# Performance work log

Hardware: AMD Instinct MI355X
Metric: run time of the kernel (lower is better)

## Reference

```python
import jax, jax.numpy as jnp
import numpy as np
import math

DIM = 512
HEADS = 8
DIM_HEAD = 64
INNER = HEADS * DIM_HEAD


def setup_inputs() -> dict:
    key = jax.random.key(0)
    k1, k2, k3, k4 = jax.random.split(key, 4)
    x = jax.random.normal(k1, (8, 1024, DIM), dtype=jnp.float32)
    w_qkv = jax.random.normal(k2, (DIM, INNER * 3), dtype=jnp.float32) / math.sqrt(DIM)
    w_out = jax.random.normal(k3, (INNER, DIM), dtype=jnp.float32) / math.sqrt(INNER)
    temperature = jnp.array(math.log(DIM_HEAD ** -0.5), dtype=jnp.float32)
    return {"x": x, "w_qkv": w_qkv, "w_out": w_out, "temperature": temperature}


def reference(x, w_qkv, w_out, temperature):
    b, n, _ = x.shape
    qkv = x @ w_qkv  # [b, n, 3*inner]
    q, k, v = jnp.split(qkv, 3, axis=-1)
    # [b, n, h*d] -> [b, h, n, d]
    def split_heads(t):
        return t.reshape(b, n, HEADS, DIM_HEAD).transpose(0, 2, 1, 3)
    q, k, v = split_heads(q), split_heads(k), split_heads(v)
    dots = jnp.einsum('bhnd,bhmd->bhnm', q, k) * jnp.exp(temperature)
    mask_value = -jnp.finfo(dots.dtype).max
    eye = jnp.eye(n, dtype=bool)
    dots = jnp.where(eye, mask_value, dots)
    attn = jax.nn.softmax(dots, axis=-1)
    out = jnp.einsum('bhnm,bhmd->bhnd', attn, v)
    out = out.transpose(0, 2, 1, 3).reshape(b, n, INNER)
    return out @ w_out
```

## Files before the change

kernel.cpp:

```cpp
#include <hip/hip_runtime.h>
#include <math.h>

#define BATCH  8
#define SEQ    1024
#define DMODEL 512
#define NHEADS 8
#define DHEAD  64
#define MTOT   (BATCH*SEQ)
#define QKVLD  (3*DMODEL)

typedef unsigned short ushortT;
typedef __attribute__((ext_vector_type(8))) short short8;
typedef __attribute__((ext_vector_type(4))) float f32x4;

typedef __attribute__((address_space(3))) unsigned char lds_byte;
typedef __attribute__((address_space(1))) const unsigned char glob_byte;

__device__ inline void g2l16(const void* g, void* l) {
    __builtin_amdgcn_global_load_lds((glob_byte*)g, (lds_byte*)l, 16, 0, 0);
}

__device__ inline ushortT f2bf(float f) {
    union { float f; unsigned u; } v; v.f = f;
    unsigned r = (v.u + 0x7FFFu + ((v.u >> 16) & 1u)) >> 16;
    return (ushortT)r;
}
__device__ inline ushortT f2bf_fast(float f) {
    union { float f; unsigned u; } v; v.f = f;
    return (ushortT)((v.u + 0x8000u) >> 16);
}

__global__ __launch_bounds__(256)
void cvt_bf16(const float* __restrict__ in, ushortT* __restrict__ out, int n8)
{
    int gid = blockIdx.x * 256 + threadIdx.x;
    if (gid >= n8) return;
    const float4 a = *(const float4*)(in + (long)gid*8);
    const float4 b = *(const float4*)(in + (long)gid*8 + 4);
    ushortT o[8];
    o[0]=f2bf(a.x); o[1]=f2bf(a.y); o[2]=f2bf(a.z); o[3]=f2bf(a.w);
    o[4]=f2bf(b.x); o[5]=f2bf(b.y); o[6]=f2bf(b.z); o[7]=f2bf(b.w);
    *(short8*)(out + (long)gid*8) = *(short8*)o;
}

__global__ __launch_bounds__(256)
void cvt_transpose2(const float* __restrict__ Wq, ushortT* __restrict__ WqT,
                    const float* __restrict__ Wo, ushortT* __restrict__ WoT)
{
    __shared__ float T[32][33];
    const int t = threadIdx.x;
    int bid = blockIdx.x;
    const float* W; ushortT* WT; int N, n0, k0;
    if (bid < 768) { W = Wq; WT = WqT; N = QKVLD;  n0 = (bid % 48) * 32; k0 = (bid / 48) * 32; }
    else { bid -= 768; W = Wo; WT = WoT; N = DMODEL; n0 = (bid % 16) * 32; k0 = (bid / 16) * 32; }
    const int K = DMODEL;
    {
        const int r = t >> 3, c4 = (t & 7) * 4;
        const float4 v = *(const float4*)(W + (long)(k0 + r)*N + n0 + c4);
        T[c4+0][r] = v.x; T[c4+1][r] = v.y; T[c4+2][r] = v.z; T[c4+3][r] = v.w;
    }
    __syncthreads();
    {
        const int n = t >> 3, k4 = (t & 7) * 4;
        ushortT o[4];
        o[0] = f2bf(T[n][k4+0]); o[1] = f2bf(T[n][k4+1]);
        o[2] = f2bf(T[n][k4+2]); o[3] = f2bf(T[n][k4+3]);
        *(uint2*)(WT + (long)(n0 + n)*K + k0 + k4) = *(uint2*)o;
    }
}

template <int MODE>
__global__ __launch_bounds__(256, 3)
void gemm_bf16(const ushortT* __restrict__ A, const ushortT* __restrict__ BT,
               void* __restrict__ Cv, ushortT* __restrict__ vT,
               const float* __restrict__ temp, int M, int N, int K)
{
    __shared__ ushortT As[128*64];
    __shared__ ushortT Bs[128*64];

    const int t    = threadIdx.x;
    const int lane = t & 63;
    const int w    = t >> 6;
    const int l15  = lane & 15, l4 = lane >> 4;

    const int nwg = gridDim.x * gridDim.y;
    const int bid = blockIdx.y * gridDim.x + blockIdx.x;
    const int swz = (bid & 7) * (nwg >> 3) + (bid >> 3);
    const int bm  = swz / gridDim.x;
    const int bn  = swz % gridDim.x;

    const int srow = t >> 3;
    const int slot = t & 7;

    f32x4 acc[4][4] = {};

    for (int kt = 0; kt < K; kt += 64) {
#pragma unroll
        for (int c = 0; c < 4; ++c) {
            const int row  = c*32 + srow;
            const int scol = ((slot ^ (row & 7)) << 4);
            g2l16((const char*)(A  + (long)(bm*128 + row)*K + kt) + scol,
                  (char*)As + c*4096 + t*16);
            g2l16((const char*)(BT + (long)(bn*128 + row)*K + kt) + scol,
                  (char*)Bs + c*4096 + t*16);
        }
        asm volatile("s_waitcnt vmcnt(0)" ::: "memory");
        __syncthreads();

#pragma unroll
        for (int kk = 0; kk < 2; ++kk) {
            short8 a[4], b[4];
#pragma unroll
            for (int i = 0; i < 4; ++i) {
                const int ra = (w >> 1)*64 + i*16 + l15;
                const int ca = (kk*32 + l4*8) ^ ((ra & 7) << 3);
                a[i] = *(const short8*)&As[ra*64 + ca];
                const int rb = (w & 1)*64 + i*16 + l15;
                const int cb = (kk*32 + l4*8) ^ ((rb & 7) << 3);
                b[i] = *(const short8*)&Bs[rb*64 + cb];
            }
#pragma unroll
            for (int i = 0; i < 4; ++i)
#pragma unroll
                for (int j = 0; j < 4; ++j)
                    acc[i][j] = __builtin_amdgcn_mfma_f32_16x16x32_bf16(
                                    a[i], b[j], acc[i][j], 0, 0, 0);
        }
        __syncthreads();
    }

    if (MODE == 1 && bn >= 8) {
#pragma unroll
        for (int i = 0; i < 4; ++i) {
            const int row0 = bm*128 + (w >> 1)*64 + i*16 + l4*4;
            const int bb   = row0 >> 10, n = row0 & 1023;
#pragma unroll
            for (int j = 0; j < 4; ++j) {
                const int cg = bn*128 + (w & 1)*64 + j*16 + l15 - 1024;
                const int h = cg >> 6, d = cg & 63;
                union { ushortT u[4]; uint2 q; } pk;
#pragma unroll
                for (int r = 0; r < 4; ++r) pk.u[r] = f2bf(acc[i][j][r]);
                *(uint2*)&vT[((long)((bb*8 + h)*64 + d))*1024 + n] = pk.q;
            }
        }
        return;
    }

    const float qs = (MODE == 1) ? __expf(temp[0]) * 1.44269504f : 1.0f;
    const float mulv = (MODE == 1 && bn < 4) ? qs : 1.0f;

#pragma unroll
    for (int i = 0; i < 4; ++i) {
        const int row0 = bm*128 + (w >> 1)*64 + i*16 + l4*4;
#pragma unroll
        for (int j = 0; j < 4; ++j) {
            const int col = bn*128 + (w & 1)*64 + j*16 + l15;
#pragma unroll
            for (int r = 0; r < 4; ++r) {
                const float v = acc[i][j][r] * mulv;
                if (MODE == 1) ((ushortT*)Cv)[(long)(row0 + r)*N + col] = f2bf(v);
                else           ((float*)Cv)[(long)(row0 + r)*N + col]   = v;
            }
        }
    }
}

__global__ __launch_bounds__(256, 3)
void attn_mfma(const ushortT* __restrict__ qkv, const ushortT* __restrict__ vT,
               ushortT* __restrict__ aout)
{
    __shared__ ushortT Ps[128*64];
    __shared__ ushortT Ks[2][64*64];
    __shared__ ushortT Vs[2][64*64];

    const int t    = threadIdx.x;
    const int lane = t & 63;
    const int w    = t >> 6;
    const int l15  = lane & 15, l4 = lane >> 4;
    const int bh   = blockIdx.x;
    const int qb   = blockIdx.y;
    const int b    = bh >> 3, h = bh & 7;

    const long row0 = (long)b * SEQ * QKVLD;
    const char* vtb = (const char*)(vT + (long)bh * 64 * 1024);

    short8 onesf;
#pragma unroll
    for (int e = 0; e < 8; ++e) onesf[e] = (short)0x3F80;

    {
        const char* qbase = (const char*)(qkv + row0 + (long)qb*128*QKVLD + h*DHEAD);
        const char* kbase = (const char*)(qkv + row0 + DMODEL + h*DHEAD);
#pragma unroll
        for (int c = 0; c < 4; ++c) {
            const int row  = c*32 + (t >> 3);
            const int scol = ((t & 7) ^ (row & 7)) << 4;
            g2l16(qbase + (long)row*(QKVLD*2) + scol, (char*)Ps + c*4096 + t*16);
        }
#pragma unroll
        for (int c = 0; c < 2; ++c) {
            const int row  = c*32 + (t >> 3);
            const int scol = ((t & 7) ^ (row & 7)) << 4;
            g2l16(kbase + (long)row*(QKVLD*2) + scol, (char*)&Ks[0][0] + c*4096 + t*16);
            g2l16(vtb + (long)row*2048 + scol,        (char*)&Vs[0][0] + c*4096 + t*16);
        }
        asm volatile("s_waitcnt vmcnt(0)" ::: "memory");
        __syncthreads();
    }

    short8 qa[2][2];
#pragma unroll
    for (int i = 0; i < 2; ++i)
#pragma unroll
    for (int kk = 0; kk < 2; ++kk) {
        const int r = w*32 + i*16 + l15;
        const int c = (kk*32 + l4*8) ^ ((r & 7) << 3);
        qa[i][kk] = *(const short8*)&Ps[r*64 + c];
    }

    f32x4 o_[2][4] = {};
    f32x4 lacc[2]  = {};

    for (int jt = 0; jt < 16; ++jt) {
        const int cur = jt & 1, nxt = cur ^ 1;
        const bool pf = (jt + 1) < 16;

        if (pf) {
            const char* kbase = (const char*)(qkv + row0 + (long)(jt+1)*64*QKVLD
                                              + DMODEL + h*DHEAD);
#pragma unroll
            for (int c = 0; c < 2; ++c) {
                const int row  = c*32 + (t >> 3);
                const int scol = ((t & 7) ^ (row & 7)) << 4;
                g2l16(kbase + (long)row*(QKVLD*2) + scol,
                      (char*)&Ks[nxt][0] + c*4096 + t*16);
                g2l16(vtb + (long)row*2048 + (jt+1)*128 + scol,
                      (char*)&Vs[nxt][0] + c*4096 + t*16);
            }
        }

        f32x4 s_[2][4] = {};
#pragma unroll
        for (int kk = 0; kk < 2; ++kk) {
            short8 kb[4];
#pragma unroll
            for (int j = 0; j < 4; ++j) {
                const int r = j*16 + l15;
                const int c = (kk*32 + l4*8) ^ ((r & 7) << 3);
                kb[j] = *(const short8*)&Ks[cur][r*64 + c];
            }
#pragma unroll
            for (int i = 0; i < 2; ++i)
#pragma unroll
            for (int j = 0; j < 4; ++j)
                s_[i][j] = __builtin_amdgcn_mfma_f32_16x16x32_bf16(
                               qa[i][kk], kb[j], s_[i][j], 0, 0, 0);
        }

        if ((jt >> 1) == qb) {
            const int coff = (jt & 1) << 6;
#pragma unroll
            for (int i = 0; i < 2; ++i)
#pragma unroll
            for (int r = 0; r < 4; ++r) {
                const int lrow = w*32 + i*16 + l4*4 + r;
#pragma unroll
                for (int j = 0; j < 4; ++j) {
                    float p = exp2f(s_[i][j][r]);
                    if (coff + j*16 + l15 == lrow) p = 0.f;
                    Ps[lrow*64 + ((j*16 + l15) ^ ((lrow & 7) << 3))] = f2bf_fast(p);
                }
            }
        } else {
#pragma unroll
            for (int i = 0; i < 2; ++i)
#pragma unroll
            for (int r = 0; r < 4; ++r) {
                const int lrow = w*32 + i*16 + l4*4 + r;
#pragma unroll
                for (int j = 0; j < 4; ++j) {
                    const float p = exp2f(s_[i][j][r]);
                    Ps[lrow*64 + ((j*16 + l15) ^ ((lrow & 7) << 3))] = f2bf_fast(p);
                }
            }
        }

#pragma unroll
        for (int kk = 0; kk < 2; ++kk) {
            short8 pa[2];
#pragma unroll
            for (int i = 0; i < 2; ++i) {
                const int rp = w*32 + i*16 + l15;
                const int cp = (kk*32 + l4*8) ^ ((rp & 7) << 3);
                pa[i] = *(const short8*)&Ps[rp*64 + cp];
                lacc[i] = __builtin_amdgcn_mfma_f32_16x16x32_bf16(
                              pa[i], onesf, lacc[i], 0, 0, 0);
            }
            short8 vb[4];
#pragma unroll
            for (int j = 0; j < 4; ++j) {
                const int r = j*16 + l15;
                const int c = (kk*32 + l4*8) ^ ((r & 7) << 3);
                vb[j] = *(const short8*)&Vs[cur][r*64 + c];
            }
#pragma unroll
            for (int i = 0; i < 2; ++i)
#pragma unroll
            for (int j = 0; j < 4; ++j)
                o_[i][j] = __builtin_amdgcn_mfma_f32_16x16x32_bf16(
                               pa[i], vb[j], o_[i][j], 0, 0, 0);
        }

        if (pf) asm volatile("s_waitcnt vmcnt(0)" ::: "memory");
        __syncthreads();
    }

#pragma unroll
    for (int i = 0; i < 2; ++i)
#pragma unroll
    for (int r = 0; r < 4; ++r) {
        const float inv  = 1.0f / lacc[i][r];
        const long  grow = (long)b*SEQ + qb*128 + w*32 + i*16 + l4*4 + r;
#pragma unroll
        for (int j = 0; j < 4; ++j)
            aout[grow*DMODEL + h*DHEAD + j*16 + l15] = f2bf(o_[i][j][r] * inv);
    }
}

extern "C" void kernel_launch(void* const* d_in, const int* in_sizes, int n_in,
                              void* d_out, int out_size, void* d_ws, size_t ws_size,
                              hipStream_t stream)
{
    const float* x     = (const float*)d_in[0];
    const float* w_qkv = (const float*)d_in[1];
    const float* w_out = (const float*)d_in[2];
    const float* temp  = (const float*)d_in[3];
    float* out = (float*)d_out;

    char* ws = (char*)d_ws;
    ushortT* x_bf   = (ushortT*)(ws);
    ushortT* wqkvT  = (ushortT*)(ws + 8388608);
    ushortT* woutT  = (ushortT*)(ws + 9961472);
    ushortT* qkv_bf = (ushortT*)(ws + 10485760);
    ushortT* vT     = (ushortT*)(ws + 35651584);
    ushortT* aout   = (ushortT*)(ws + 44040192);

    cvt_bf16<<<dim3((MTOT*DMODEL/8)/256), 256, 0, stream>>>(x, x_bf, MTOT*DMODEL/8);
    cvt_transpose2<<<dim3(1024), 256, 0, stream>>>(w_qkv, wqkvT, w_out, woutT);

    gemm_bf16<1><<<dim3(QKVLD/128, MTOT/128), 256, 0, stream>>>(
        x_bf, wqkvT, qkv_bf, vT, temp, MTOT, QKVLD, DMODEL);

    attn_mfma<<<dim3(BATCH*NHEADS, SEQ/128), 256, 0, stream>>>(qkv_bf, vT, aout);

    gemm_bf16<0><<<dim3(DMODEL/128, MTOT/128), 256, 0, stream>>>(
        aout, woutT, out, nullptr, nullptr, MTOT, DMODEL, DMODEL);
}
```

Measured before the change: 141.0 us.

## Double-buffer GEMM LDS tiles, merge conversion kernels, change P-tile swizzle

The GEMM now double-buffers its A/B LDS tiles, issuing async global-to-LDS loads for the next K slice while MFMAs run on the current one, and occupancy is lowered to 2 waves per SIMD to fit the doubled LDS. The x conversion and the weight transpose/convert kernels are merged into one launch to save a kernel launch. The attention P-tile LDS swizzle is changed to a different XOR pattern meant to reduce bank conflicts on writes and reads. Risks are lower occupancy in the GEMM and the new swizzle possibly conflicting more on the read side.

```diff
diff --git a/kernel.cpp b/kernel.cpp
--- a/kernel.cpp
+++ b/kernel.cpp
@@ -31,25 +31,24 @@
 }
 
 __global__ __launch_bounds__(256)
-void cvt_bf16(const float* __restrict__ in, ushortT* __restrict__ out, int n8)
-{
-    int gid = blockIdx.x * 256 + threadIdx.x;
-    if (gid >= n8) return;
-    const float4 a = *(const float4*)(in + (long)gid*8);
-    const float4 b = *(const float4*)(in + (long)gid*8 + 4);
-    ushortT o[8];
-    o[0]=f2bf(a.x); o[1]=f2bf(a.y); o[2]=f2bf(a.z); o[3]=f2bf(a.w);
-    o[4]=f2bf(b.x); o[5]=f2bf(b.y); o[6]=f2bf(b.z); o[7]=f2bf(b.w);
-    *(short8*)(out + (long)gid*8) = *(short8*)o;
-}
-
-__global__ __launch_bounds__(256)
-void cvt_transpose2(const float* __restrict__ Wq, ushortT* __restrict__ WqT,
-                    const float* __restrict__ Wo, ushortT* __restrict__ WoT)
+void cvt_all(const float* __restrict__ x, ushortT* __restrict__ x_bf,
+             const float* __restrict__ Wq, ushortT* __restrict__ WqT,
+             const float* __restrict__ Wo, ushortT* __restrict__ WoT)
 {
     __shared__ float T[32][33];
     const int t = threadIdx.x;
     int bid = blockIdx.x;
+    if (bid < 2048) {
+        const int gid = bid * 256 + t;
+        const float4 a = *(const float4*)(x + (long)gid*8);
+        const float4 b = *(const float4*)(x + (long)gid*8 + 4);
+        ushortT o[8];
+        o[0]=f2bf(a.x); o[1]=f2bf(a.y); o[2]=f2bf(a.z); o[3]=f2bf(a.w);
+        o[4]=f2bf(b.x); o[5]=f2bf(b.y); o[6]=f2bf(b.z); o[7]=f2bf(b.w);
+        *(short8*)(x_bf + (long)gid*8) = *(short8*)o;
+        return;
+    }
+    bid -= 2048;
     const float* W; ushortT* WT; int N, n0, k0;
     if (bid < 768) { W = Wq; WT = WqT; N = QKVLD;  n0 = (bid % 48) * 32; k0 = (bid / 48) * 32; }
     else { bid -= 768; W = Wo; WT = WoT; N = DMODEL; n0 = (bid % 16) * 32; k0 = (bid / 16) * 32; }
@@ -70,13 +69,13 @@
 }
 
 template <int MODE>
-__global__ __launch_bounds__(256, 3)
+__global__ __launch_bounds__(256, 2)
 void gemm_bf16(const ushortT* __restrict__ A, const ushortT* __restrict__ BT,
                void* __restrict__ Cv, ushortT* __restrict__ vT,
                const float* __restrict__ temp, int M, int N, int K)
 {
-    __shared__ ushortT As[128*64];
-    __shared__ ushortT Bs[128*64];
+    __shared__ ushortT As[2][128*64];
+    __shared__ ushortT Bs[2][128*64];
 
     const int t    = threadIdx.x;
     const int lane = t & 63;
@@ -93,20 +92,38 @@
     const int slot = t & 7;
 
     f32x4 acc[4][4] = {};
-
-    for (int kt = 0; kt < K; kt += 64) {
-#pragma unroll
-        for (int c = 0; c < 4; ++c) {
-            const int row  = c*32 + srow;
-            const int scol = ((slot ^ (row & 7)) << 4);
-            g2l16((const char*)(A  + (long)(bm*128 + row)*K + kt) + scol,
-                  (char*)As + c*4096 + t*16);
-            g2l16((const char*)(BT + (long)(bn*128 + row)*K + kt) + scol,
-                  (char*)Bs + c*4096 + t*16);
-        }
-        asm volatile("s_waitcnt vmcnt(0)" ::: "memory");
-        __syncthreads();
-
+    const int NK = K >> 6;
+
+#pragma unroll
+    for (int c = 0; c < 4; ++c) {
+        const int row  = c*32 + srow;
+        const int scol = ((slot ^ (row & 7)) << 4);
+        g2l16((const char*)(A  + (long)(bm*128 + row)*K) + scol,
+              (char*)&As[0][0] + c*4096 + t*16);
+        g2l16((const char*)(BT + (long)(bn*128 + row)*K) + scol,
+              (char*)&Bs[0][0] + c*4096 + t*16);
+    }
+    asm volatile("s_waitcnt vmcnt(0)" ::: "memory");
+    __syncthreads();
+
+    for (int it = 0; it < NK; ++it) {
+        const int cur = it & 1;
+
+        if (it + 1 < NK) {
+            const int kt = (it + 1) << 6;
+#pragma unroll
+            for (int c = 0; c < 4; ++c) {
+                const int row  = c*32 + srow;
+                const int scol = ((slot ^ (row & 7)) << 4);
+                g2l16((const char*)(A  + (long)(bm*128 + row)*K + kt) + scol,
+                      (char*)&As[cur^1][0] + c*4096 + t*16);
+                g2l16((const char*)(BT + (long)(bn*128 + row)*K + kt) + scol,
+                      (char*)&Bs[cur^1][0] + c*4096 + t*16);
+            }
+        }
+
+        const ushortT* Ac = &As[cur][0];
+        const ushortT* Bc = &Bs[cur][0];
 #pragma unroll
         for (int kk = 0; kk < 2; ++kk) {
             short8 a[4], b[4];
@@ -114,10 +131,10 @@
             for (int i = 0; i < 4; ++i) {
                 const int ra = (w >> 1)*64 + i*16 + l15;
                 const int ca = (kk*32 + l4*8) ^ ((ra & 7) << 3);
-                a[i] = *(const short8*)&As[ra*64 + ca];
+                a[i] = *(const short8*)&Ac[ra*64 + ca];
                 const int rb = (w & 1)*64 + i*16 + l15;
                 const int cb = (kk*32 + l4*8) ^ ((rb & 7) << 3);
-                b[i] = *(const short8*)&Bs[rb*64 + cb];
+                b[i] = *(const short8*)&Bc[rb*64 + cb];
             }
 #pragma unroll
             for (int i = 0; i < 4; ++i)
@@ -126,6 +143,8 @@
                     acc[i][j] = __builtin_amdgcn_mfma_f32_16x16x32_bf16(
                                     a[i], b[j], acc[i][j], 0, 0, 0);
         }
+
+        asm volatile("s_waitcnt vmcnt(0)" ::: "memory");
         __syncthreads();
     }
 
@@ -269,7 +288,7 @@
                 for (int j = 0; j < 4; ++j) {
                     float p = exp2f(s_[i][j][r]);
                     if (coff + j*16 + l15 == lrow) p = 0.f;
-                    Ps[lrow*64 + ((j*16 + l15) ^ ((lrow & 7) << 3))] = f2bf_fast(p);
+                    Ps[lrow*64 + ((j*16 + l15) ^ (((lrow >> 2) & 3) << 4))] = f2bf_fast(p);
                 }
             }
         } else {
@@ -281,7 +300,7 @@
 #pragma unroll
                 for (int j = 0; j < 4; ++j) {
                     const float p = exp2f(s_[i][j][r]);
-                    Ps[lrow*64 + ((j*16 + l15) ^ ((lrow & 7) << 3))] = f2bf_fast(p);
+                    Ps[lrow*64 + ((j*16 + l15) ^ (((lrow >> 2) & 3) << 4))] = f2bf_fast(p);
                 }
             }
         }
@@ -292,7 +311,7 @@
 #pragma unroll
             for (int i = 0; i < 2; ++i) {
                 const int rp = w*32 + i*16 + l15;
-                const int cp = (kk*32 + l4*8) ^ ((rp & 7) << 3);
+                const int cp = (kk*32 + l4*8) ^ (((rp >> 2) & 3) << 4);
                 pa[i] = *(const short8*)&Ps[rp*64 + cp];
                 lacc[i] = __builtin_amdgcn_mfma_f32_16x16x32_bf16(
                               pa[i], onesf, lacc[i], 0, 0, 0);
@@ -346,8 +365,7 @@
     ushortT* vT     = (ushortT*)(ws + 35651584);
     ushortT* aout   = (ushortT*)(ws + 44040192);
 
-    cvt_bf16<<<dim3((MTOT*DMODEL/8)/256), 256, 0, stream>>>(x, x_bf, MTOT*DMODEL/8);
-    cvt_transpose2<<<dim3(1024), 256, 0, stream>>>(w_qkv, wqkvT, w_out, woutT);
+    cvt_all<<<dim3(3072), 256, 0, stream>>>(x, x_bf, w_qkv, wqkvT, w_out, woutT);
 
     gemm_bf16<1><<<dim3(QKVLD/128, MTOT/128), 256, 0, stream>>>(
         x_bf, wqkvT, qkv_bf, vT, temp, MTOT, QKVLD, DMODEL);
```

Result: slower. 148.9 us (+5.6%).
